# Optimization experiments

Measured on AMD Instinct MI355X. Metric: run time of the kernel, lower is better.

## Reference

```python
import jax, jax.numpy as jnp
import numpy as np

DIM = 256        # word / relation / entity-type embedding dim
STATEDIM = 256   # agent state dim
VOCAB = 100000
REL_COUNT = 25
T = 128          # sentence length


def _lstm(wvs, Wih, Whh, bih, bhh, reverse):
    # PyTorch LSTMCell gate order: i, f, g, o
    def step(carry, x):
        h, c = carry
        g = x @ Wih.T + bih + h @ Whh.T + bhh
        i, f, gg, o = jnp.split(g, 4)
        c = jax.nn.sigmoid(f) * c + jax.nn.sigmoid(i) * jnp.tanh(gg)
        h = jax.nn.sigmoid(o) * jnp.tanh(c)
        return (h, c), h
    init = (jnp.zeros((DIM,), jnp.float32), jnp.zeros((DIM,), jnp.float32))
    _, hs = jax.lax.scan(step, init, wvs, reverse=reverse)
    return hs


def setup_inputs() -> dict:
    key = jax.random.key(0)
    ks = jax.random.split(key, 32)
    def p(i, shape, scale=0.05):
        return (jax.random.normal(ks[i], shape) * scale).astype(jnp.float32)
    return {
        "text": jax.random.randint(ks[0], (T,), 0, VOCAB, dtype=jnp.int32),
        "wordvector": p(1, (VOCAB, DIM)),
        "relvec": p(2, (REL_COUNT + 1, DIM)),
        "entvec": p(3, (7, DIM)),
        "WihL": p(4, (4 * DIM, DIM)), "WhhL": p(5, (4 * DIM, DIM)),
        "bihL": p(6, (4 * DIM,)), "bhhL": p(7, (4 * DIM,)),
        "WihR": p(8, (4 * DIM, DIM)), "WhhR": p(9, (4 * DIM, DIM)),
        "bihR": p(10, (4 * DIM,)), "bhhR": p(11, (4 * DIM,)),
        "Wt": p(12, (STATEDIM, 3 * DIM + STATEDIM)), "bt": p(13, (STATEDIM,)),
        "Wp": p(14, (REL_COUNT + 1, STATEDIM)), "bp": p(15, (REL_COUNT + 1,)),
        "Wb": p(16, (STATEDIM, 3 * DIM + 2 * STATEDIM)), "bb": p(17, (STATEDIM,)),
        "Wpl": p(18, (REL_COUNT, 7, STATEDIM)), "bpl": p(19, (REL_COUNT, 7)),
        "Wtt": p(20, (STATEDIM, STATEDIM)), "btt": p(21, (STATEDIM,)),
        "Wtb": p(22, (STATEDIM, STATEDIM)), "btb": p(23, (STATEDIM,)),
        "Wbt": p(24, (STATEDIM, STATEDIM)), "bbt": p(25, (STATEDIM,)),
    }


def reference(text, wordvector, relvec, entvec, WihL, WhhL, bihL, bhhL,
              WihR, WhhR, bihR, bhhR, Wt, bt, Wp, bp, Wb, bb, Wpl, bpl,
              Wtt, btt, Wtb, btb, Wbt, bbt):
    # mode = "test_NER": deterministic argmax sampling, dropout disabled.
    wvs = wordvector[text]                               # [T, DIM]
    front = _lstm(wvs, WihL, WhhL, bihL, bhhL, False)    # [T, DIM]
    back = _lstm(wvs, WihR, WhhR, bihR, bhhR, True)      # [T, DIM]
    wordin = jnp.concatenate([front, back], axis=1)      # [T, 2*DIM]

    def bot_rollout(rel_idx, target, memb0):
        Wr, br = Wpl[rel_idx], bpl[rel_idx]              # per-relation head
        def stepb(carry, w):
            memb, ab = carry
            inpb = jnp.concatenate([w, entvec[ab], memb, target])
            outb = jnp.tanh(inpb @ Wb.T + bb)            # dropout off (test)
            probb = jax.nn.softmax(outb @ Wr.T + br)
            ab2 = jnp.argmax(probb).astype(jnp.int32)
            return (outb, ab2), (ab2, probb[ab2])
        (membf, _), (acts, aps) = jax.lax.scan(
            stepb, (memb0, jnp.zeros((), jnp.int32)), wordin)
        return membf, acts, aps

    def top_step(carry, w):
        mem, rel_action = carry
        inp = jnp.concatenate([w, relvec[rel_action], mem])
        outp = jnp.tanh(inp @ Wt.T + bt)                 # dropout off (test)
        prob = jax.nn.softmax(outp @ Wp.T + bp)
        action = jnp.argmax(prob).astype(jnp.int32)
        actprob = prob[action]
        do_ner = action > 0
        rel_next = jnp.where(do_ner, action, rel_action)
        rel_idx = jnp.maximum(action, 1) - 1
        target = outp @ Wtt.T + btt
        memb0 = outp @ Wtb.T + btb
        membf, acts, aps = bot_rollout(rel_idx, target, memb0)
        mem_after = membf @ Wbt.T + bbt
        mem_next = jnp.where(do_ner, mem_after, outp)
        acts = jnp.where(do_ner, acts, 0)
        aps = jnp.where(do_ner, aps, 0.0)
        return (mem_next, rel_next), (action, actprob, acts, aps)

    init = (jnp.zeros((STATEDIM,), jnp.float32), jnp.zeros((), jnp.int32))
    _, (top_actions, top_actprobs, bot_actions, bot_actprobs) = jax.lax.scan(
        top_step, init, wordin)
    # bot rows where no NER sub-rollout fired are zero-filled (orig: empty lists)
    return top_actions, top_actprobs, bot_actions, bot_actprobs
```

## Files before the change

### kernel.cpp

```cpp
#include <hip/hip_runtime.h>
#include <float.h>

constexpr int SEQ  = 128;
constexpr int D    = 256;
constexpr int G    = 1024;
constexpr int NREL = 26;
constexpr int NENT = 7;

typedef float v2f __attribute__((ext_vector_type(2)));

__global__ void k_trans(const float* __restrict__ in, float* __restrict__ out,
                        int rows, int cols, int in_stride, int in_off)
{
    int idx = blockIdx.x * 256 + threadIdx.x;
    if (idx >= rows * cols) return;
    int i = idx % rows;
    int k = idx / rows;
    out[idx] = in[(size_t)i * in_stride + in_off + k];
}

__global__ __launch_bounds__(1024) void k_xg(
    const int* __restrict__ text, const float* __restrict__ wv,
    const float* __restrict__ Wih, const float* __restrict__ bih,
    const float* __restrict__ bhh, float* __restrict__ xg)
{
    int t = blockIdx.x, j = threadIdx.x;
    const float* x  = wv + (size_t)text[t] * D;
    const float* wr = Wih + (size_t)j * D;
    float acc = bih[j] + bhh[j];
    for (int k = 0; k < D; ++k) acc += x[k] * wr[k];
    xg[t * G + j] = acc;
}

__global__ __launch_bounds__(1024) void k_lstm(
    const float* __restrict__ xgF, const float* __restrict__ xgB,
    const float* __restrict__ WHTF, const float* __restrict__ WHTB,
    float* __restrict__ wordin)
{
    int dir = blockIdx.x;
    const float* xg  = dir ? xgB  : xgF;
    const float* WHT = dir ? WHTB : WHTF;
    __shared__ float h[D], c[D], g[G];
    int j = threadIdx.x;
    if (j < D) { h[j] = 0.f; c[j] = 0.f; }
    __syncthreads();
    for (int s = 0; s < SEQ; ++s) {
        int t = dir ? (SEQ - 1 - s) : s;
        float acc = xg[t * G + j];
        for (int k = 0; k < D; ++k) acc += WHT[k * G + j] * h[k];
        g[j] = acc;
        __syncthreads();
        if (j < D) {
            float si = 1.f / (1.f + expf(-g[j]));
            float sf = 1.f / (1.f + expf(-g[D + j]));
            float gg = tanhf(g[2 * D + j]);
            float so = 1.f / (1.f + expf(-g[3 * D + j]));
            float cn = sf * c[j] + si * gg;
            float hn = so * tanhf(cn);
            c[j] = cn; h[j] = hn;
            wordin[t * (2 * D) + dir * D + j] = hn;
        }
        __syncthreads();
    }
}

__global__ __launch_bounds__(256) void k_prep2(
    const float* __restrict__ wordin,
    const float* __restrict__ WTWT, const float* __restrict__ WBWT,
    const float* __restrict__ WTRT, const float* __restrict__ WBET,
    const float* __restrict__ relvec, const float* __restrict__ entvec,
    const float* __restrict__ btv, const float* __restrict__ bbv,
    float* __restrict__ TW, float* __restrict__ BW,
    float* __restrict__ RV, float* __restrict__ EV)
{
    int b = blockIdx.x, i = threadIdx.x;
    if (b < SEQ) {
        const float* w = wordin + b * (2 * D);
        float a1 = btv[i], a2 = bbv[i];
        for (int j = 0; j < 2 * D; ++j) {
            float wv = w[j];
            a1 += wv * WTWT[j * D + i];
            a2 += wv * WBWT[j * D + i];
        }
        TW[b * D + i] = a1;
        BW[b * D + i] = a2;
    } else if (b < SEQ + NREL) {
        int r = b - SEQ;
        const float* x = relvec + r * D;
        float a = 0.f;
        for (int k = 0; k < D; ++k) a += x[k] * WTRT[k * D + i];
        RV[r * D + i] = a;
    } else {
        int e = b - SEQ - NREL;
        const float* x = entvec + e * D;
        float a = 0.f;
        for (int k = 0; k < D; ++k) a += x[k] * WBET[k * D + i];
        EV[e * D + i] = a;
    }
}

__global__ __launch_bounds__(256) void k_m1(
    const float* __restrict__ WBGT, const float* __restrict__ Wtt,
    float* __restrict__ M1T)
{
    int j = blockIdx.x, i = threadIdx.x;
    float a = 0.f;
    for (int k = 0; k < D; ++k) a = fmaf(WBGT[k * D + i], Wtt[k * D + j], a);
    M1T[j * D + i] = a;
}

__global__ __launch_bounds__(256) void k_c1(
    const float* __restrict__ WBGT, const float* __restrict__ btt,
    float* __restrict__ c1)
{
    int i = threadIdx.x;
    float a = 0.f;
    for (int k = 0; k < D; ++k) a = fmaf(WBGT[k * D + i], btt[k], a);
    c1[i] = a;
}

__global__ __launch_bounds__(256) void k_pack(
    const float* __restrict__ Wb, float* __restrict__ WB2)
{
    int e = blockIdx.x * 256 + threadIdx.x;
    int tid = e >> 7, kk = e & 127;
    int h = tid >> 8, i = tid & 255;
    WB2[e] = Wb[(size_t)i * (5 * D) + 3 * D + h * 128 + kk];
}

__device__ inline float mv_half(const float* __restrict__ Wcol,
                                const float* __restrict__ x)
{
    float a0 = 0.f, a1 = 0.f, a2 = 0.f, a3 = 0.f;
    #pragma unroll
    for (int kk = 0; kk < 128; kk += 4) {
        a0 = fmaf(Wcol[(kk + 0) * D], x[kk + 0], a0);
        a1 = fmaf(Wcol[(kk + 1) * D], x[kk + 1], a1);
        a2 = fmaf(Wcol[(kk + 2) * D], x[kk + 2], a2);
        a3 = fmaf(Wcol[(kk + 3) * D], x[kk + 3], a3);
    }
    return (a0 + a1) + (a2 + a3);
}

template<int W>
__device__ inline void grp_smax(float lv, int n, int lane, int& am, float& pm)
{
    float mx = lv;
    #pragma unroll
    for (int off = W / 2; off; off >>= 1) mx = fmaxf(mx, __shfl_xor(mx, off));
    float e  = (lane < n) ? expf(lv - mx) : 0.f;
    float se = e;
    #pragma unroll
    for (int off = W / 2; off; off >>= 1) se += __shfl_xor(se, off);
    float p  = (lane < n) ? (e / se) : -1.f;
    float q  = p;
    #pragma unroll
    for (int off = W / 2; off; off >>= 1) q = fmaxf(q, __shfl_xor(q, off));
    unsigned long long mask = __ballot(p == q);
    am = __ffsll((long long)mask) - 1;
    pm = q;
}

__global__ __launch_bounds__(512, 2) void k_main2(
    const float* __restrict__ TW,   const float* __restrict__ BW,
    const float* __restrict__ RV,   const float* __restrict__ EV,
    const float* __restrict__ WTMT, const float* __restrict__ WTBT,
    const float* __restrict__ WBTT, const float* __restrict__ M1T,
    const float* __restrict__ c1v,  const float* __restrict__ WB2,
    const float* __restrict__ Wp,   const float* __restrict__ bp,
    const float* __restrict__ Wpl,  const float* __restrict__ bpl,
    const float* __restrict__ btb,  const float* __restrict__ bbt,
    float* __restrict__ out)
{
    const int tid  = threadIdx.x;
    const int lane = tid & 63;
    const int wv   = tid >> 6;
    const int h    = tid >> 8;
    const int i    = tid & 255;
    const bool lower = (tid < 256);

    __shared__ __align__(16) float xbuf[2][D];
    __shared__ __align__(16) float pbuf[D], pbufB[D], pbufC[D];
    __shared__ __align__(16) float mem[D], outv[D];
    __shared__ __align__(16) float WrSh[NENT * D];
    __shared__ float lpart[4][32];
    __shared__ float brSh[8];

    v2f w2[64];
    {
        const v2f* src = reinterpret_cast<const v2f*>(WB2) + tid * 64;
        #pragma unroll
        for (int q = 0; q < 64; ++q) w2[q] = src[q];
    }
    float ev0 = 0.f, ev1 = 0.f, ev2 = 0.f, ev3 = 0.f,
          ev4 = 0.f, ev5 = 0.f, ev6 = 0.f;
    if (lower) {
        ev0 = EV[0 * D + i]; ev1 = EV[1 * D + i]; ev2 = EV[2 * D + i];
        ev3 = EV[3 * D + i]; ev4 = EV[4 * D + i]; ev5 = EV[5 * D + i];
        ev6 = EV[6 * D + i];
        mem[i] = 0.f;
    }
    __syncthreads();

    const float* WTMh = WTMT + (size_t)h * 128 * D + i;
    const float* WTBh = WTBT + (size_t)h * 128 * D + i;
    const float* WBTh = WBTT + (size_t)h * 128 * D + i;
    const float* M1h  = M1T  + (size_t)h * 128 * D + i;

    int rel = 0;

    for (int t = 0; t < SEQ; ++t) {
        float a = mv_half(WTMh, mem + h * 128);
        if (!lower) pbuf[i] = a;
        __syncthreads();
        if (lower) {
            float tot  = a + pbuf[i] + TW[t * D + i] + RV[rel * D + i];
            float outp = tanhf(tot);
            outv[i] = outp;
            #pragma unroll
            for (int r = 0; r < NREL; ++r) {
                float pp = outp * Wp[r * D + i];
                #pragma unroll
                for (int off = 32; off; off >>= 1) pp += __shfl_xor(pp, off);
                if (lane == 0) lpart[wv][r] = pp;
            }
        }
        __syncthreads();
        float lv = -FLT_MAX;
        if (lane < NREL)
            lv = lpart[0][lane] + lpart[1][lane] + lpart[2][lane] +
                 lpart[3][lane] + bp[lane];
        int am; float pm;
        grp_smax<32>(lv, NREL, lane, am, pm);
        if (tid == 0) { out[t] = (float)am; out[SEQ + t] = pm; }
        const int action = am;

        if (action > 0) {
            rel = action;
            float bs = mv_half(WTBh, outv + h * 128);
            float cs = mv_half(M1h,  outv + h * 128);
            if (!lower) { pbufB[i] = bs; pbufC[i] = cs; }
            const size_t wbase = (size_t)(action - 1) * NENT * D;
            for (int k = tid; k < NENT * D; k += 512) WrSh[k] = Wpl[wbase + k];
            if (tid < NENT) brSh[tid] = bpl[(action - 1) * NENT + tid];
            __syncthreads();
            float btm = 0.f, bwc = 0.f;
            if (lower) {
                xbuf[0][i] = bs + pbufB[i] + btb[i];
                btm = cs + pbufC[i] + c1v[i];
                bwc = BW[i];
            }
            __syncthreads();

            int p = 0, ab = 0;
            for (int s = 0; s < SEQ; ++s) {
                const float4* xb =
                    reinterpret_cast<const float4*>(xbuf[p] + h * 128);
                v2f A0 = {0.f, 0.f}, A1 = {0.f, 0.f},
                    A2 = {0.f, 0.f}, A3 = {0.f, 0.f};
                #pragma unroll
                for (int q = 0; q < 32; q += 2) {
                    float4 x0 = xb[q], x1 = xb[q + 1];
                    v2f xa = {x0.x, x0.y}, xc = {x0.z, x0.w};
                    v2f xd = {x1.x, x1.y}, xe = {x1.z, x1.w};
                    A0 = __builtin_elementwise_fma(w2[2 * q + 0], xa, A0);
                    A1 = __builtin_elementwise_fma(w2[2 * q + 1], xc, A1);
                    A2 = __builtin_elementwise_fma(w2[2 * q + 2], xd, A2);
                    A3 = __builtin_elementwise_fma(w2[2 * q + 3], xe, A3);
                }
                float ms = ((A0.x + A0.y) + (A1.x + A1.y)) +
                           ((A2.x + A2.y) + (A3.x + A3.y));
                if (!lower) pbuf[i] = ms;
                __syncthreads();
                if (lower) {
                    float ev = (ab == 0) ? ev0 : (ab == 1) ? ev1 :
                               (ab == 2) ? ev2 : (ab == 3) ? ev3 :
                               (ab == 4) ? ev4 : (ab == 5) ? ev5 : ev6;
                    float tot = ms + pbuf[i] + bwc + ev + btm;
                    float ob = tanhf(tot);
                    xbuf[p ^ 1][i] = ob;
                    #pragma unroll
                    for (int r = 0; r < NENT; ++r) {
                        float pp = ob * WrSh[r * D + i];
                        #pragma unroll
                        for (int off = 32; off; off >>= 1)
                            pp += __shfl_xor(pp, off);
                        if (lane == 0) lpart[wv][r] = pp;
                    }
                    int sn = (s + 1 < SEQ) ? s + 1 : s;
                    bwc = BW[sn * D + i];
                }
                __syncthreads();
                float lv2 = -FLT_MAX;
                if (lane < NENT)
                    lv2 = lpart[0][lane] + lpart[1][lane] + lpart[2][lane] +
                          lpart[3][lane] + brSh[lane];
                int am2; float pm2;
                grp_smax<8>(lv2, NENT, lane, am2, pm2);
                if (tid == 0) {
                    out[2 * SEQ + t * SEQ + s] = (float)am2;
                    out[2 * SEQ + SEQ * SEQ + t * SEQ + s] = pm2;
                }
                ab = am2;
                p ^= 1;
            }
            float es = mv_half(WBTh, xbuf[p] + h * 128);
            if (!lower) pbuf[i] = es;
            __syncthreads();
            if (lower) mem[i] = es + pbuf[i] + bbt[i];
            __syncthreads();
        } else {
            if (lower) mem[i] = outv[i];
            if (tid < SEQ) {
                out[2 * SEQ + t * SEQ + tid] = 0.f;
                out[2 * SEQ + SEQ * SEQ + t * SEQ + tid] = 0.f;
            }
            __syncthreads();
        }
    }
}

extern "C" void kernel_launch(void* const* d_in, const int* in_sizes, int n_in,
                              void* d_out, int out_size, void* d_ws, size_t ws_size,
                              hipStream_t stream)
{
    (void)in_sizes; (void)n_in; (void)out_size; (void)ws_size;
    const int*   text       = (const int*)  d_in[0];
    const float* wordvector = (const float*)d_in[1];
    const float* relvec     = (const float*)d_in[2];
    const float* entvec     = (const float*)d_in[3];
    const float* WihL = (const float*)d_in[4];  const float* WhhL = (const float*)d_in[5];
    const float* bihL = (const float*)d_in[6];  const float* bhhL = (const float*)d_in[7];
    const float* WihR = (const float*)d_in[8];  const float* WhhR = (const float*)d_in[9];
    const float* bihR = (const float*)d_in[10]; const float* bhhR = (const float*)d_in[11];
    const float* Wt   = (const float*)d_in[12]; const float* bt   = (const float*)d_in[13];
    const float* Wp   = (const float*)d_in[14]; const float* bp   = (const float*)d_in[15];
    const float* Wb   = (const float*)d_in[16]; const float* bb   = (const float*)d_in[17];
    const float* Wpl  = (const float*)d_in[18]; const float* bpl  = (const float*)d_in[19];
    const float* Wtt  = (const float*)d_in[20]; const float* btt  = (const float*)d_in[21];
    const float* Wtb  = (const float*)d_in[22]; const float* btb  = (const float*)d_in[23];
    const float* Wbt  = (const float*)d_in[24]; const float* bbt  = (const float*)d_in[25];

    float* ws = (float*)d_ws;
    size_t o = 0;
    auto take = [&](size_t n) { float* p = ws + o; o += n; return p; };
    float* XGF    = take(SEQ * G);
    float* XGB    = take(SEQ * G);
    float* WHLT   = take(D * G);
    float* WHRT   = take(D * G);
    float* WORDIN = take(SEQ * 2 * D);
    float* TW     = take(SEQ * D);
    float* BW     = take(SEQ * D);
    float* RVb    = take(NREL * D);
    float* EVb    = take(NENT * D);
    float* WTWT   = take(2 * D * D);
    float* WTRT   = take(D * D);
    float* WTMT   = take(D * D);
    float* WBWT   = take(2 * D * D);
    float* WBET   = take(D * D);
    float* WBGT   = take(D * D);
    float* WTBT   = take(D * D);
    float* WBTT   = take(D * D);
    float* M1T    = take(D * D);
    float* C1     = take(D);
    float* WB2    = take(2 * 128 * D);

    auto tr = [&](const float* in, float* outp, int rows, int cols, int stride, int off) {
        int n = rows * cols;
        k_trans<<<(n + 255) / 256, 256, 0, stream>>>(in, outp, rows, cols, stride, off);
    };
    tr(WhhL, WHLT, G, D, D, 0);
    tr(WhhR, WHRT, G, D, D, 0);
    tr(Wt,  WTWT, D, 2 * D, G, 0);
    tr(Wt,  WTRT, D, D, G, 512);
    tr(Wt,  WTMT, D, D, G, 768);
    tr(Wb,  WBWT, D, 2 * D, 5 * D, 0);
    tr(Wb,  WBET, D, D, 5 * D, 512);
    tr(Wb,  WBGT, D, D, 5 * D, 1024);
    tr(Wtb, WTBT, D, D, D, 0);
    tr(Wbt, WBTT, D, D, D, 0);

    k_m1<<<D, D, 0, stream>>>(WBGT, Wtt, M1T);
    k_c1<<<1, D, 0, stream>>>(WBGT, btt, C1);
    k_pack<<<256, 256, 0, stream>>>(Wb, WB2);

    k_xg<<<SEQ, 1024, 0, stream>>>(text, wordvector, WihL, bihL, bhhL, XGF);
    k_xg<<<SEQ, 1024, 0, stream>>>(text, wordvector, WihR, bihR, bhhR, XGB);
    k_lstm<<<2, 1024, 0, stream>>>(XGF, XGB, WHLT, WHRT, WORDIN);
    k_prep2<<<SEQ + NREL + NENT, 256, 0, stream>>>(WORDIN, WTWT, WBWT, WTRT, WBET,
                                                   relvec, entvec, bt, bb,
                                                   TW, BW, RVb, EVb);
    k_main2<<<1, 512, 0, stream>>>(TW, BW, RVb, EVb, WTMT, WTBT, WBTT, M1T, C1,
                                   WB2, Wp, bp, Wpl, bpl, btb, bbt,
                                   (float*)d_out);
}
```

Before: 60.78 ms.

## Split main recurrent kernel K-dimension across four quarters with 1024 threads

The single-block sequential kernel now uses 1024 threads instead of 512, splitting each 256-long matrix-vector dot product into four 64-element quarters. Each thread holds half as many register-resident weights, and the partial sums are combined through four shared-memory rows. The goal is to shorten the serial per-step dot-product latency in the 128x128 nested rollout. In exchange, every step does more cross-wave reduction work and synchronises across 16 waves instead of 8, and an inline-asm barrier is added to pin the weights in registers.

```diff
diff --git a/kernel.cpp b/kernel.cpp
--- a/kernel.cpp
+++ b/kernel.cpp
@@ -119,21 +119,21 @@
     c1[i] = a;
 }
 
-__global__ __launch_bounds__(256) void k_pack(
-    const float* __restrict__ Wb, float* __restrict__ WB2)
+__global__ __launch_bounds__(256) void k_pack4(
+    const float* __restrict__ Wb, float* __restrict__ WB4)
 {
     int e = blockIdx.x * 256 + threadIdx.x;
-    int tid = e >> 7, kk = e & 127;
-    int h = tid >> 8, i = tid & 255;
-    WB2[e] = Wb[(size_t)i * (5 * D) + 3 * D + h * 128 + kk];
-}
-
-__device__ inline float mv_half(const float* __restrict__ Wcol,
-                                const float* __restrict__ x)
+    int tid = e >> 6, kk = e & 63;
+    int q = tid >> 8, i = tid & 255;
+    WB4[e] = Wb[(size_t)i * (5 * D) + 3 * D + q * 64 + kk];
+}
+
+__device__ inline float mv_q(const float* __restrict__ Wcol,
+                             const float* __restrict__ x)
 {
     float a0 = 0.f, a1 = 0.f, a2 = 0.f, a3 = 0.f;
     #pragma unroll
-    for (int kk = 0; kk < 128; kk += 4) {
+    for (int kk = 0; kk < 64; kk += 4) {
         a0 = fmaf(Wcol[(kk + 0) * D], x[kk + 0], a0);
         a1 = fmaf(Wcol[(kk + 1) * D], x[kk + 1], a1);
         a2 = fmaf(Wcol[(kk + 2) * D], x[kk + 2], a2);
@@ -161,12 +161,13 @@
     pm = q;
 }
 
-__global__ __launch_bounds__(512, 2) void k_main2(
+__global__ __launch_bounds__(1024, 4)
+void k_main3(
     const float* __restrict__ TW,   const float* __restrict__ BW,
     const float* __restrict__ RV,   const float* __restrict__ EV,
     const float* __restrict__ WTMT, const float* __restrict__ WTBT,
     const float* __restrict__ WBTT, const float* __restrict__ M1T,
-    const float* __restrict__ c1v,  const float* __restrict__ WB2,
+    const float* __restrict__ c1v,  const float* __restrict__ WB4,
     const float* __restrict__ Wp,   const float* __restrict__ bp,
     const float* __restrict__ Wpl,  const float* __restrict__ bpl,
     const float* __restrict__ btb,  const float* __restrict__ bbt,
@@ -174,23 +175,33 @@
 {
     const int tid  = threadIdx.x;
     const int lane = tid & 63;
-    const int wv   = tid >> 6;
-    const int h    = tid >> 8;
+    const int lwv  = (tid >> 6) & 3;
+    const int q    = tid >> 8;
     const int i    = tid & 255;
     const bool lower = (tid < 256);
 
     __shared__ __align__(16) float xbuf[2][D];
-    __shared__ __align__(16) float pbuf[D], pbufB[D], pbufC[D];
+    __shared__ __align__(16) float psA[4][D], psB[4][D];
     __shared__ __align__(16) float mem[D], outv[D];
     __shared__ __align__(16) float WrSh[NENT * D];
     __shared__ float lpart[4][32];
     __shared__ float brSh[8];
 
-    v2f w2[64];
+    v2f w2[32];
     {
-        const v2f* src = reinterpret_cast<const v2f*>(WB2) + tid * 64;
+        const float4* src = reinterpret_cast<const float4*>(WB4) + tid * 16;
         #pragma unroll
-        for (int q = 0; q < 64; ++q) w2[q] = src[q];
+        for (int k4 = 0; k4 < 16; ++k4) {
+            float4 v = src[k4];
+            w2[2 * k4 + 0] = (v2f){v.x, v.y};
+            w2[2 * k4 + 1] = (v2f){v.z, v.w};
+        }
+    }
+    #pragma unroll
+    for (int k2 = 0; k2 < 32; ++k2) {
+        double dp = __builtin_bit_cast(double, w2[k2]);
+        asm volatile("" : "+v"(dp));
+        w2[k2] = __builtin_bit_cast(v2f, dp);
     }
     float ev0 = 0.f, ev1 = 0.f, ev2 = 0.f, ev3 = 0.f,
           ev4 = 0.f, ev5 = 0.f, ev6 = 0.f;
@@ -202,19 +213,19 @@
     }
     __syncthreads();
 
-    const float* WTMh = WTMT + (size_t)h * 128 * D + i;
-    const float* WTBh = WTBT + (size_t)h * 128 * D + i;
-    const float* WBTh = WBTT + (size_t)h * 128 * D + i;
-    const float* M1h  = M1T  + (size_t)h * 128 * D + i;
+    const float* WTMq = WTMT + (size_t)q * 64 * D + i;
+    const float* WTBq = WTBT + (size_t)q * 64 * D + i;
+    const float* WBTq = WBTT + (size_t)q * 64 * D + i;
+    const float* M1q  = M1T  + (size_t)q * 64 * D + i;
 
     int rel = 0;
 
     for (int t = 0; t < SEQ; ++t) {
-        float a = mv_half(WTMh, mem + h * 128);
-        if (!lower) pbuf[i] = a;
+        psA[q][i] = mv_q(WTMq, mem + q * 64);
         __syncthreads();
         if (lower) {
-            float tot  = a + pbuf[i] + TW[t * D + i] + RV[rel * D + i];
+            float tot = psA[0][i] + psA[1][i] + psA[2][i] + psA[3][i] +
+                        TW[t * D + i] + RV[rel * D + i];
             float outp = tanhf(tot);
             outv[i] = outp;
             #pragma unroll
@@ -222,7 +233,7 @@
                 float pp = outp * Wp[r * D + i];
                 #pragma unroll
                 for (int off = 32; off; off >>= 1) pp += __shfl_xor(pp, off);
-                if (lane == 0) lpart[wv][r] = pp;
+                if (lane == 0) lpart[lwv][r] = pp;
             }
         }
         __syncthreads();
@@ -237,17 +248,17 @@
 
         if (action > 0) {
             rel = action;
-            float bs = mv_half(WTBh, outv + h * 128);
-            float cs = mv_half(M1h,  outv + h * 128);
-            if (!lower) { pbufB[i] = bs; pbufC[i] = cs; }
+            psA[q][i] = mv_q(WTBq, outv + q * 64);
+            psB[q][i] = mv_q(M1q,  outv + q * 64);
             const size_t wbase = (size_t)(action - 1) * NENT * D;
-            for (int k = tid; k < NENT * D; k += 512) WrSh[k] = Wpl[wbase + k];
+            for (int k = tid; k < NENT * D; k += 1024) WrSh[k] = Wpl[wbase + k];
             if (tid < NENT) brSh[tid] = bpl[(action - 1) * NENT + tid];
             __syncthreads();
             float btm = 0.f, bwc = 0.f;
             if (lower) {
-                xbuf[0][i] = bs + pbufB[i] + btb[i];
-                btm = cs + pbufC[i] + c1v[i];
+                xbuf[0][i] = psA[0][i] + psA[1][i] + psA[2][i] + psA[3][i] +
+                             btb[i];
+                btm = psB[0][i] + psB[1][i] + psB[2][i] + psB[3][i] + c1v[i];
                 bwc = BW[i];
             }
             __syncthreads();
@@ -255,28 +266,32 @@
             int p = 0, ab = 0;
             for (int s = 0; s < SEQ; ++s) {
                 const float4* xb =
-                    reinterpret_cast<const float4*>(xbuf[p] + h * 128);
+                    reinterpret_cast<const float4*>(xbuf[p] + q * 64);
                 v2f A0 = {0.f, 0.f}, A1 = {0.f, 0.f},
                     A2 = {0.f, 0.f}, A3 = {0.f, 0.f};
                 #pragma unroll
-                for (int q = 0; q < 32; q += 2) {
-                    float4 x0 = xb[q], x1 = xb[q + 1];
-                    v2f xa = {x0.x, x0.y}, xc = {x0.z, x0.w};
-                    v2f xd = {x1.x, x1.y}, xe = {x1.z, x1.w};
-                    A0 = __builtin_elementwise_fma(w2[2 * q + 0], xa, A0);
-                    A1 = __builtin_elementwise_fma(w2[2 * q + 1], xc, A1);
-                    A2 = __builtin_elementwise_fma(w2[2 * q + 2], xd, A2);
-                    A3 = __builtin_elementwise_fma(w2[2 * q + 3], xe, A3);
+                for (int k4 = 0; k4 < 16; k4 += 4) {
+                    float4 x0 = xb[k4], x1 = xb[k4 + 1],
+                           x2 = xb[k4 + 2], x3 = xb[k4 + 3];
+                    A0 = __builtin_elementwise_fma(w2[2 * k4 + 0], (v2f){x0.x, x0.y}, A0);
+                    A0 = __builtin_elementwise_fma(w2[2 * k4 + 1], (v2f){x0.z, x0.w}, A0);
+                    A1 = __builtin_elementwise_fma(w2[2 * k4 + 2], (v2f){x1.x, x1.y}, A1);
+                    A1 = __builtin_elementwise_fma(w2[2 * k4 + 3], (v2f){x1.z, x1.w}, A1);
+                    A2 = __builtin_elementwise_fma(w2[2 * k4 + 4], (v2f){x2.x, x2.y}, A2);
+                    A2 = __builtin_elementwise_fma(w2[2 * k4 + 5], (v2f){x2.z, x2.w}, A2);
+                    A3 = __builtin_elementwise_fma(w2[2 * k4 + 6], (v2f){x3.x, x3.y}, A3);
+                    A3 = __builtin_elementwise_fma(w2[2 * k4 + 7], (v2f){x3.z, x3.w}, A3);
                 }
-                float ms = ((A0.x + A0.y) + (A1.x + A1.y)) +
-                           ((A2.x + A2.y) + (A3.x + A3.y));
-                if (!lower) pbuf[i] = ms;
+                v2f AS = (A0 + A1) + (A2 + A3);
+                float ms = AS.x + AS.y;
+                psA[q][i] = ms;
                 __syncthreads();
                 if (lower) {
                     float ev = (ab == 0) ? ev0 : (ab == 1) ? ev1 :
                                (ab == 2) ? ev2 : (ab == 3) ? ev3 :
                                (ab == 4) ? ev4 : (ab == 5) ? ev5 : ev6;
-                    float tot = ms + pbuf[i] + bwc + ev + btm;
+                    float tot = ms + psA[1][i] + psA[2][i] + psA[3][i] +
+                                bwc + ev + btm;
                     float ob = tanhf(tot);
                     xbuf[p ^ 1][i] = ob;
                     #pragma unroll
@@ -285,7 +300,7 @@
                         #pragma unroll
                         for (int off = 32; off; off >>= 1)
                             pp += __shfl_xor(pp, off);
-                        if (lane == 0) lpart[wv][r] = pp;
+                        if (lane == 0) lpart[lwv][r] = pp;
                     }
                     int sn = (s + 1 < SEQ) ? s + 1 : s;
                     bwc = BW[sn * D + i];
@@ -304,10 +319,11 @@
                 ab = am2;
                 p ^= 1;
             }
-            float es = mv_half(WBTh, xbuf[p] + h * 128);
-            if (!lower) pbuf[i] = es;
+            psA[q][i] = mv_q(WBTq, xbuf[p] + q * 64);
             __syncthreads();
-            if (lower) mem[i] = es + pbuf[i] + bbt[i];
+            if (lower)
+                mem[i] = psA[0][i] + psA[1][i] + psA[2][i] + psA[3][i] +
+                         bbt[i];
             __syncthreads();
         } else {
             if (lower) mem[i] = outv[i];
@@ -363,7 +379,7 @@
     float* WBTT   = take(D * D);
     float* M1T    = take(D * D);
     float* C1     = take(D);
-    float* WB2    = take(2 * 128 * D);
+    float* WB4    = take(1024 * 64);
 
     auto tr = [&](const float* in, float* outp, int rows, int cols, int stride, int off) {
         int n = rows * cols;
@@ -382,7 +398,7 @@
 
     k_m1<<<D, D, 0, stream>>>(WBGT, Wtt, M1T);
     k_c1<<<1, D, 0, stream>>>(WBGT, btt, C1);
-    k_pack<<<256, 256, 0, stream>>>(Wb, WB2);
+    k_pack4<<<256, 256, 0, stream>>>(Wb, WB4);
 
     k_xg<<<SEQ, 1024, 0, stream>>>(text, wordvector, WihL, bihL, bhhL, XGF);
     k_xg<<<SEQ, 1024, 0, stream>>>(text, wordvector, WihR, bihR, bhhR, XGB);
@@ -390,7 +406,7 @@
     k_prep2<<<SEQ + NREL + NENT, 256, 0, stream>>>(WORDIN, WTWT, WBWT, WTRT, WBET,
                                                    relvec, entvec, bt, bb,
                                                    TW, BW, RVb, EVb);
-    k_main2<<<1, 512, 0, stream>>>(TW, BW, RVb, EVb, WTMT, WTBT, WBTT, M1T, C1,
-                                   WB2, Wp, bp, Wpl, bpl, btb, bbt,
-                                   (float*)d_out);
-}
+    k_main3<<<1, 1024, 0, stream>>>(TW, BW, RVb, EVb, WTMT, WTBT, WBTT, M1T, C1,
+                                    WB4, Wp, bp, Wpl, bpl, btb, bbt,
+                                    (float*)d_out);
+}
```

Result: faster. 57.85 ms (-4.8%).
